# Optimization experiments

Hardware: AMD Instinct MI355X
Metric: run time of the kernel (lower is better)

Reference implementation:

```python
import jax, jax.numpy as jnp
import numpy as np

N_NODES = 100000
N_EDGES = 1600000
FEAT = 64
HIDDEN = 64
NUM_GRAPHS = 64


def gcn_conv(x, row, col, norm, W, b, n_nodes):
    # x: [N, in], W: [in, out]; PyG GCNConv: transform, then normalized scatter-add, then bias
    xw = x @ W                                   # [N, out]
    msgs = xw[row] * norm[:, None]               # [E+N, out]
    out = jax.ops.segment_sum(msgs, col, num_segments=n_nodes)
    return out + b


def _norm_and_loops(edge_index, n_nodes):
    # add self loops and compute symmetric normalization deg^-1/2 * deg^-1/2
    loop = jnp.arange(n_nodes, dtype=edge_index.dtype)
    row = jnp.concatenate([edge_index[0], loop])  # sources
    col = jnp.concatenate([edge_index[1], loop])  # targets
    ew = jnp.ones(row.shape[0], dtype=jnp.float32)
    deg = jax.ops.segment_sum(ew, col, num_segments=n_nodes)
    dinv = jnp.where(deg > 0, jax.lax.rsqrt(jnp.maximum(deg, 1.0)), 0.0)
    norm = dinv[row] * dinv[col]
    return row, col, norm


def setup_inputs() -> dict:
    key = jax.random.key(0)
    ks = jax.random.split(key, 10)
    x = jax.random.normal(ks[0], (N_NODES, FEAT), dtype=jnp.float32)
    edge_index = jax.random.randint(ks[1], (2, N_EDGES), 0, N_NODES, dtype=jnp.int64 if jax.config.jax_enable_x64 else jnp.int32)
    batch = jnp.sort(jax.random.randint(ks[2], (N_NODES,), 0, NUM_GRAPHS, dtype=edge_index.dtype))
    def xavier(k, fan_in, fan_out):
        lim = np.sqrt(6.0 / (fan_in + fan_out))
        return jax.random.uniform(k, (fan_in, fan_out), minval=-lim, maxval=lim, dtype=jnp.float32)
    W1 = xavier(ks[3], FEAT, HIDDEN)
    W2 = xavier(ks[4], HIDDEN, HIDDEN)
    W3 = xavier(ks[5], HIDDEN, HIDDEN)
    b1 = jnp.zeros((HIDDEN,), jnp.float32)
    b2 = jnp.zeros((HIDDEN,), jnp.float32)
    b3 = jnp.zeros((HIDDEN,), jnp.float32)
    return {"x": x, "edge_index": edge_index, "batch": batch,
            "W1": W1, "b1": b1, "W2": W2, "b2": b2, "W3": W3, "b3": b3}


def reference(x, edge_index, batch, W1, b1, W2, b2, W3, b3):
    n_nodes = x.shape[0]
    row, col, norm = _norm_and_loops(edge_index, n_nodes)
    xs = []
    h = x
    for W, b in ((W1, b1), (W2, b2), (W3, b3)):
        h = gcn_conv(h, row, col, norm, W, b, n_nodes)
        h = jax.nn.relu(h)
        xs.append(h)
    # global_add_pool per layer, then concat along features -> [num_graphs, 3*hidden]
    pooled = [jax.ops.segment_sum(h, batch, num_segments=NUM_GRAPHS) for h in xs]
    return jnp.concatenate(pooled, axis=1)
```

## Files before the change

kernel.cpp:

```cpp
#include <hip/hip_runtime.h>


#define F 64
#define F4 (F / 4)
#define CAP 48
#define NPW 16
#define NRANGE 8

static inline size_t alignup(size_t x, size_t a) { return (x + a - 1) & ~(a - 1); }

__device__ __forceinline__ ushort f2bf(float f) {
    unsigned u = __builtin_bit_cast(unsigned, f);
    unsigned r = (u + 0x7fffu + ((u >> 16) & 1u)) >> 16;
    return (ushort)r;
}
__device__ __forceinline__ float bf2f(ushort v) {
    return __builtin_bit_cast(float, ((unsigned)v) << 16);
}
__device__ __forceinline__ float4 bf4_to_f4(ushort4 v) {
    return make_float4(bf2f(v.x), bf2f(v.y), bf2f(v.z), bf2f(v.w));
}

__global__ __launch_bounds__(256) void k_build(const int* __restrict__ rowv,
                                               const int* __restrict__ colv,
                                               int* __restrict__ cnt,
                                               int* __restrict__ csr,
                                               int E, int rsize) {
    int r = blockIdx.x & (NRANGE - 1);
    int e4 = (blockIdx.x >> 3) * 256 + threadIdx.x;
    int lo = r * rsize;
    int hiEx = lo + rsize;
    int E4 = E >> 2;
    if (e4 < E4) {
        int4 c = ((const int4*)colv)[e4];
        int4 s = ((const int4*)rowv)[e4];
        int p;
        if (c.x >= lo && c.x < hiEx) {
            p = atomicAdd(&cnt[c.x], 1);
            if (p < CAP) csr[(size_t)c.x * CAP + p] = s.x;
        }
        if (c.y >= lo && c.y < hiEx) {
            p = atomicAdd(&cnt[c.y], 1);
            if (p < CAP) csr[(size_t)c.y * CAP + p] = s.y;
        }
        if (c.z >= lo && c.z < hiEx) {
            p = atomicAdd(&cnt[c.z], 1);
            if (p < CAP) csr[(size_t)c.z * CAP + p] = s.z;
        }
        if (c.w >= lo && c.w < hiEx) {
            p = atomicAdd(&cnt[c.w], 1);
            if (p < CAP) csr[(size_t)c.w * CAP + p] = s.w;
        }
    }
    int tail = E & 3;
    if (r == 0 && (int)blockIdx.x < NRANGE && (int)threadIdx.x < tail) {
        int e = (E4 << 2) + threadIdx.x;
        int c = colv[e], s = rowv[e];
        int p = atomicAdd(&cnt[c], 1);
        if (p < CAP) csr[(size_t)c * CAP + p] = s;
    }
}

template <typename T>
__global__ __launch_bounds__(256) void k_gemm(const T* __restrict__ H,
                                              const float* __restrict__ W,
                                              const int* __restrict__ cnt,
                                              ushort* __restrict__ XW, int n) {
    __shared__ float wl[F * F];
    __shared__ float hl[64][F];
    for (int t = threadIdx.x; t < F * F4; t += 256)
        ((float4*)wl)[t] = ((const float4*)W)[t];
    __syncthreads();
    int c = threadIdx.x & 63;
    int rg = threadIdx.x >> 6;
    float wc[F];
#pragma unroll
    for (int k = 0; k < F; ++k) wc[k] = wl[k * F + c];

    int rowBase = blockIdx.x * 64;
    for (int t = threadIdx.x; t < 64 * 16; t += 256) {
        int r = t >> 4;
        int kc = (t & 15) << 2;
        int gr = rowBase + r;
        float4 v = make_float4(0.f, 0.f, 0.f, 0.f);
        if (gr < n) {
            if constexpr (sizeof(T) == 4) {
                v = ((const float4*)H)[(size_t)gr * F4 + (kc >> 2)];
            } else {
                ushort4 u = ((const ushort4*)H)[(size_t)gr * F4 + (kc >> 2)];
                v = bf4_to_f4(u);
            }
        }
        *(float4*)&hl[r][kc] = v;
    }
    __syncthreads();

    for (int rr = 0; rr < 16; ++rr) {
        int r = rg + (rr << 2);
        float acc = 0.f;
#pragma unroll
        for (int k = 0; k < F; k += 4) {
            float4 h4 = *(const float4*)&hl[r][k];
            acc = fmaf(h4.x, wc[k], acc);
            acc = fmaf(h4.y, wc[k + 1], acc);
            acc = fmaf(h4.z, wc[k + 2], acc);
            acc = fmaf(h4.w, wc[k + 3], acc);
        }
        int gr = rowBase + r;
        if (gr < n) XW[(size_t)gr * F + c] = f2bf(acc * rsqrtf((float)cnt[gr] + 1.0f));
    }
}

__global__ __launch_bounds__(256) void k_gather(const ushort* __restrict__ XW,
                                                const int* __restrict__ cnt,
                                                const int* __restrict__ csr,
                                                const float* __restrict__ bias,
                                                ushort* __restrict__ h,
                                                int n) {
    int lane = threadIdx.x & 63;
    int q = lane >> 4, s = lane & 15;
    int wave = blockIdx.x * (blockDim.x >> 6) + (threadIdx.x >> 6);
    int base = wave * NPW;
    if (base >= n) return;
    float4 bv = ((const float4*)bias)[s];
    const ushort4* XW4 = (const ushort4*)XW;
    for (int t = 0; t < NPW / 4; ++t) {
        int node = base + (t << 2) + q;
        if (node >= n) continue;
        int deg = cnt[node];
        const int* cr = csr + (size_t)node * CAP;
        float4 sum = bf4_to_f4(XW4[(size_t)node * 16 + s]);
        int j = 0;
        for (; j + 4 <= deg; j += 4) {
            int4 a = *(const int4*)(cr + j);
            float4 v0 = bf4_to_f4(XW4[(size_t)a.x * 16 + s]);
            float4 v1 = bf4_to_f4(XW4[(size_t)a.y * 16 + s]);
            float4 v2 = bf4_to_f4(XW4[(size_t)a.z * 16 + s]);
            float4 v3 = bf4_to_f4(XW4[(size_t)a.w * 16 + s]);
            sum.x += (v0.x + v1.x) + (v2.x + v3.x);
            sum.y += (v0.y + v1.y) + (v2.y + v3.y);
            sum.z += (v0.z + v1.z) + (v2.z + v3.z);
            sum.w += (v0.w + v1.w) + (v2.w + v3.w);
        }
        for (; j < deg; ++j) {
            float4 v = bf4_to_f4(XW4[(size_t)cr[j] * 16 + s]);
            sum.x += v.x; sum.y += v.y; sum.z += v.z; sum.w += v.w;
        }
        float sc = rsqrtf((float)deg + 1.0f);
        ushort4 hv;
        hv.x = f2bf(fmaxf(fmaf(sum.x, sc, bv.x), 0.f));
        hv.y = f2bf(fmaxf(fmaf(sum.y, sc, bv.y), 0.f));
        hv.z = f2bf(fmaxf(fmaf(sum.z, sc, bv.z), 0.f));
        hv.w = f2bf(fmaxf(fmaf(sum.w, sc, bv.w), 0.f));
        ((ushort4*)h)[(size_t)node * 16 + s] = hv;
    }
}

__global__ __launch_bounds__(256) void k_pool(const ushort* __restrict__ h,
                                              const int* __restrict__ batch,
                                              float* __restrict__ out,
                                              int layerOff, int n) {
    __shared__ int se[2];
    __shared__ float part[4][F];
    int g = blockIdx.x;
    if (threadIdx.x == 0) {
        int lo = 0, hi = n;
        while (lo < hi) { int mid = (lo + hi) >> 1; if (batch[mid] < g) lo = mid + 1; else hi = mid; }
        se[0] = lo;
        hi = n;
        while (lo < hi) { int mid = (lo + hi) >> 1; if (batch[mid] < g + 1) lo = mid + 1; else hi = mid; }
        se[1] = lo;
    }
    __syncthreads();
    int start = se[0], end = se[1];
    int f = threadIdx.x & 63;
    int w = threadIdx.x >> 6;
    float s0 = 0.f, s1 = 0.f, s2 = 0.f, s3 = 0.f;
    int node = start + w;
    for (; node + 12 < end; node += 16) {
        s0 += bf2f(h[(size_t)node * F + f]);
        s1 += bf2f(h[(size_t)(node + 4) * F + f]);
        s2 += bf2f(h[(size_t)(node + 8) * F + f]);
        s3 += bf2f(h[(size_t)(node + 12) * F + f]);
    }
    for (; node < end; node += 4) s0 += bf2f(h[(size_t)node * F + f]);
    part[w][f] = (s0 + s1) + (s2 + s3);
    __syncthreads();
    if (threadIdx.x < F) {
        float t = part[0][f] + part[1][f] + part[2][f] + part[3][f];
        out[g * (3 * F) + layerOff + f] = t;
    }
}

extern "C" void kernel_launch(void* const* d_in, const int* in_sizes, int n_in,
                              void* d_out, int out_size, void* d_ws, size_t ws_size,
                              hipStream_t stream) {
    const float* x = (const float*)d_in[0];
    const int* edge = (const int*)d_in[1];
    const int* batch = (const int*)d_in[2];
    const float* Ws[3] = {(const float*)d_in[3], (const float*)d_in[5], (const float*)d_in[7]};
    const float* bs[3] = {(const float*)d_in[4], (const float*)d_in[6], (const float*)d_in[8]};
    float* out = (float*)d_out;

    const int N = in_sizes[0] / F;
    const int E = in_sizes[1] / 2;
    const int* rowv = edge;
    const int* colv = edge + E;

    char* ws = (char*)d_ws;
    size_t off = 0;
    int*    cnt = (int*)(ws + off);    off = alignup(off + (size_t)N * 4, 256);
    int*    csr = (int*)(ws + off);    off = alignup(off + (size_t)N * CAP * 4, 256);
    ushort* xw  = (ushort*)(ws + off); off = alignup(off + (size_t)N * F * 2, 256);
    ushort* h   = (ushort*)(ws + off); off = alignup(off + (size_t)N * F * 2, 256);
    (void)ws_size;

    hipMemsetAsync(out, 0, (size_t)out_size * sizeof(float), stream);
    hipMemsetAsync(cnt, 0, (size_t)N * 4, stream);

    const int rsize = (N + NRANGE - 1) / NRANGE;
    const int chunks = ((E >> 2) + 255) / 256;
    k_build<<<chunks * NRANGE, 256, 0, stream>>>(rowv, colv, cnt, csr, E, rsize);

    const int gemmBlocks = (N + 63) / 64;
    const int gatherWaves = (N + NPW - 1) / NPW;
    const int gatherBlocks = (gatherWaves + 3) / 4;

    for (int l = 0; l < 3; ++l) {
        if (l == 0)
            k_gemm<float><<<gemmBlocks, 256, 0, stream>>>(x, Ws[l], cnt, xw, N);
        else
            k_gemm<ushort><<<gemmBlocks, 256, 0, stream>>>(h, Ws[l], cnt, xw, N);
        k_gather<<<gatherBlocks, 256, 0, stream>>>(xw, cnt, csr, bs[l], h, N);
        k_pool<<<64, 256, 0, stream>>>(h, batch, out, l * F, N);
    }
}
```

Measured before the change: 372.9 us.

## Use bf16 MFMA for the per-layer feature transform GEMM

Replaces the scalar FP32 FMA GEMM with a kernel built on 16x16x32 bf16 MFMA instructions, one 16-row tile per wave. Small prep kernels convert x to bf16 once and convert and transpose the three weight matrices. The goal is to cut ALU time in the transform stage. The cost is two extra launches, an extra pass over x, and bf16 rounding of the first-layer inputs and weights. The memset of the output buffer is also dropped, which is only correct if the pooling kernel writes every output element directly rather than accumulating into it.

```diff
diff --git a/kernel.cpp b/kernel.cpp
--- a/kernel.cpp
+++ b/kernel.cpp
@@ -2,10 +2,12 @@
 
 
 #define F 64
-#define F4 (F / 4)
 #define CAP 48
 #define NPW 16
 #define NRANGE 8
+
+typedef __attribute__((ext_vector_type(8))) short short8x;
+typedef __attribute__((ext_vector_type(4))) float f32x4;
 
 static inline size_t alignup(size_t x, size_t a) { return (x + a - 1) & ~(a - 1); }
 
@@ -61,53 +63,77 @@
     }
 }
 
-template <typename T>
-__global__ __launch_bounds__(256) void k_gemm(const T* __restrict__ H,
-                                              const float* __restrict__ W,
+__global__ __launch_bounds__(256) void k_prepx(const float* __restrict__ x,
+                                               ushort* __restrict__ xbf, long n4) {
+    long i = (long)blockIdx.x * 256 + threadIdx.x;
+    if (i < n4) {
+        float4 v = ((const float4*)x)[i];
+        ushort4 u;
+        u.x = f2bf(v.x); u.y = f2bf(v.y); u.z = f2bf(v.z); u.w = f2bf(v.w);
+        ((ushort4*)xbf)[i] = u;
+    }
+}
+
+__global__ __launch_bounds__(256) void k_prepw(const float* __restrict__ W0,
+                                               const float* __restrict__ W1,
+                                               const float* __restrict__ W2,
+                                               ushort* __restrict__ wt) {
+    const float* W = (blockIdx.x == 0) ? W0 : (blockIdx.x == 1) ? W1 : W2;
+    ushort* o = wt + (size_t)blockIdx.x * F * F;
+    for (int i = threadIdx.x; i < F * F; i += 256) {
+        int k = i >> 6, c = i & 63;
+        o[c * F + k] = f2bf(W[i]);
+    }
+}
+
+__global__ __launch_bounds__(256) void k_gemm(const ushort* __restrict__ Hbf,
+                                              const ushort* __restrict__ WT,
                                               const int* __restrict__ cnt,
                                               ushort* __restrict__ XW, int n) {
-    __shared__ float wl[F * F];
-    __shared__ float hl[64][F];
-    for (int t = threadIdx.x; t < F * F4; t += 256)
-        ((float4*)wl)[t] = ((const float4*)W)[t];
+    __shared__ ushort hl[64][72];
+    __shared__ ushort wl[64][72];
+    int rowBase = blockIdx.x * 64;
+    for (int i = threadIdx.x; i < 1024; i += 256) {
+        int idx = i & 511;
+        int row = idx >> 3, cb = (idx & 7) << 3;
+        if (i < 512) {
+            int gr = rowBase + row;
+            short8x v = {0, 0, 0, 0, 0, 0, 0, 0};
+            if (gr < n) v = *(const short8x*)(Hbf + (size_t)gr * F + cb);
+            *(short8x*)&hl[row][cb] = v;
+        } else {
+            *(short8x*)&wl[row][cb] = *(const short8x*)(WT + row * F + cb);
+        }
+    }
     __syncthreads();
-    int c = threadIdx.x & 63;
-    int rg = threadIdx.x >> 6;
-    float wc[F];
+
+    int lane = threadIdx.x & 63;
+    int w = threadIdx.x >> 6;
+    int l15 = lane & 15, l4 = lane >> 4;
+
+    short8x a0 = *(const short8x*)&hl[w * 16 + l15][l4 * 8];
+    short8x a1 = *(const short8x*)&hl[w * 16 + l15][32 + l4 * 8];
+
+    f32x4 acc[4];
 #pragma unroll
-    for (int k = 0; k < F; ++k) wc[k] = wl[k * F + c];
-
-    int rowBase = blockIdx.x * 64;
-    for (int t = threadIdx.x; t < 64 * 16; t += 256) {
-        int r = t >> 4;
-        int kc = (t & 15) << 2;
-        int gr = rowBase + r;
-        float4 v = make_float4(0.f, 0.f, 0.f, 0.f);
+    for (int ct = 0; ct < 4; ++ct) {
+        acc[ct] = (f32x4){0.f, 0.f, 0.f, 0.f};
+        short8x b0 = *(const short8x*)&wl[ct * 16 + l15][l4 * 8];
+        short8x b1 = *(const short8x*)&wl[ct * 16 + l15][32 + l4 * 8];
+        acc[ct] = __builtin_amdgcn_mfma_f32_16x16x32_bf16(a0, b0, acc[ct], 0, 0, 0);
+        acc[ct] = __builtin_amdgcn_mfma_f32_16x16x32_bf16(a1, b1, acc[ct], 0, 0, 0);
+    }
+
+#pragma unroll
+    for (int r = 0; r < 4; ++r) {
+        int gr = rowBase + w * 16 + l4 * 4 + r;
         if (gr < n) {
-            if constexpr (sizeof(T) == 4) {
-                v = ((const float4*)H)[(size_t)gr * F4 + (kc >> 2)];
-            } else {
-                ushort4 u = ((const ushort4*)H)[(size_t)gr * F4 + (kc >> 2)];
-                v = bf4_to_f4(u);
+            float sc = rsqrtf((float)cnt[gr] + 1.0f);
+#pragma unroll
+            for (int ct = 0; ct < 4; ++ct) {
+                XW[(size_t)gr * F + ct * 16 + l15] = f2bf(acc[ct][r] * sc);
             }
         }
-        *(float4*)&hl[r][kc] = v;
-    }
-    __syncthreads();
-
-    for (int rr = 0; rr < 16; ++rr) {
-        int r = rg + (rr << 2);
-        float acc = 0.f;
-#pragma unroll
-        for (int k = 0; k < F; k += 4) {
-            float4 h4 = *(const float4*)&hl[r][k];
-            acc = fmaf(h4.x, wc[k], acc);
-            acc = fmaf(h4.y, wc[k + 1], acc);
-            acc = fmaf(h4.z, wc[k + 2], acc);
-            acc = fmaf(h4.w, wc[k + 3], acc);
-        }
-        int gr = rowBase + r;
-        if (gr < n) XW[(size_t)gr * F + c] = f2bf(acc * rsqrtf((float)cnt[gr] + 1.0f));
     }
 }
 
@@ -213,24 +239,27 @@
     int*    csr = (int*)(ws + off);    off = alignup(off + (size_t)N * CAP * 4, 256);
     ushort* xw  = (ushort*)(ws + off); off = alignup(off + (size_t)N * F * 2, 256);
     ushort* h   = (ushort*)(ws + off); off = alignup(off + (size_t)N * F * 2, 256);
+    ushort* xbf = (ushort*)(ws + off); off = alignup(off + (size_t)N * F * 2, 256);
+    ushort* wt  = (ushort*)(ws + off); off = alignup(off + (size_t)3 * F * F * 2, 256);
     (void)ws_size;
 
-    hipMemsetAsync(out, 0, (size_t)out_size * sizeof(float), stream);
     hipMemsetAsync(cnt, 0, (size_t)N * 4, stream);
 
     const int rsize = (N + NRANGE - 1) / NRANGE;
     const int chunks = ((E >> 2) + 255) / 256;
     k_build<<<chunks * NRANGE, 256, 0, stream>>>(rowv, colv, cnt, csr, E, rsize);
 
+    const long n4 = ((long)N * F) / 4;
+    k_prepx<<<(int)((n4 + 255) / 256), 256, 0, stream>>>(x, xbf, n4);
+    k_prepw<<<3, 256, 0, stream>>>(Ws[0], Ws[1], Ws[2], wt);
+
     const int gemmBlocks = (N + 63) / 64;
     const int gatherWaves = (N + NPW - 1) / NPW;
     const int gatherBlocks = (gatherWaves + 3) / 4;
 
     for (int l = 0; l < 3; ++l) {
-        if (l == 0)
-            k_gemm<float><<<gemmBlocks, 256, 0, stream>>>(x, Ws[l], cnt, xw, N);
-        else
-            k_gemm<ushort><<<gemmBlocks, 256, 0, stream>>>(h, Ws[l], cnt, xw, N);
+        const ushort* Hin = (l == 0) ? xbf : h;
+        k_gemm<<<gemmBlocks, 256, 0, stream>>>(Hin, wt + (size_t)l * F * F, cnt, xw, N);
         k_gather<<<gatherBlocks, 256, 0, stream>>>(xw, cnt, csr, bs[l], h, N);
         k_pool<<<64, 256, 0, stream>>>(h, batch, out, l * F, N);
     }
```

Result: faster. 335.6 us (-10.0%).
